# Performance work log

Measured on AMD Instinct MI355X. Metric: run time of the kernel, lower is better.

## Reference

```python
import jax, jax.numpy as jnp
import numpy as np

IMG_H, IMG_W = 240, 320
NEAR, FAR = 0.1, 10.0
CHUNK = 64  # triangles rasterized per scan step
CAM_K = np.array([[286.2057, 0.0, 162.6306],
                  [0.0, 286.7852, 121.0245],
                  [0.0, 0.0, 1.0]], np.float32)


def build_projection(cam, w, h, x0=0, y0=0, nc=NEAR, fc=FAR):
    q = -(fc + nc) / float(fc - nc)
    qn = -2.0 * fc * nc / float(fc - nc)
    proj = np.array([
        [2 * cam[0, 0] / w, -2 * cam[0, 1] / w, (-2 * cam[0, 2] + w + 2 * x0) / w, 0],
        [0, -2 * cam[1, 1] / h, (-2 * cam[1, 2] + h + 2 * y0) / h, 0],
        [0, 0, q, qn],
        [0, 0, -1, 0]], dtype=np.float64)
    proj[1, :] *= -1.0
    return jnp.asarray(proj.T, jnp.float32)


def vertex_normals(verts, faces):
    # per-face normal scattered to its vertices then renormalized
    # (equals dirt lighting.vertex_normals_pre_split on split meshes)
    v0, v1, v2 = verts[faces[:, 0]], verts[faces[:, 1]], verts[faces[:, 2]]
    fn = jnp.cross(v1 - v0, v2 - v0)
    fn = fn / jnp.maximum(jnp.linalg.norm(fn, axis=1, keepdims=True), 1e-12)
    vn = (jnp.zeros_like(verts)
          .at[faces[:, 0]].add(fn)
          .at[faces[:, 1]].add(fn)
          .at[faces[:, 2]].add(fn))
    return vn / jnp.maximum(jnp.linalg.norm(vn, axis=1, keepdims=True), 1e-12)


def transform_vertices(vertices, pose, faces, proj):
    vert_obj = jnp.concatenate([vertices, jnp.ones_like(vertices[:, -1:])], axis=1)  # [V,4]
    normals = vertex_normals(vert_obj[:, :3], faces)
    gl = jnp.array([[1., 0., 0.], [0., -1., 0.], [0., 0., -1.]], jnp.float32)
    rot = gl @ pose[:3, :3]
    # replicate the flat-list surgery: cam_pose[:3,:3]=gl@R, negate t_y, t_z
    cam_pose = pose.at[:3, :3].set(rot).at[1, 3].multiply(-1.0).at[2, 3].multiply(-1.0)
    view = cam_pose.T
    vert_cam = vert_obj @ view                                   # [V,4]
    vert_3d = vert_obj[:, :3] @ pose[:3, :3].T + pose[:3, 3]     # [V,3]
    vert_clip = vert_cam @ proj                                  # [V,4]
    return vert_obj, vert_3d, vert_clip, normals


def rasterise(vert_clip, colors, faces, H, W):
    # z-buffered triangle rasterization with perspective-correct barycentric
    # interpolation, processed in chunks of CHUNK triangles via lax.scan.
    eps = 1e-9
    wc = vert_clip[:, 3]
    inv_w = 1.0 / jnp.where(jnp.abs(wc) > eps, wc, eps)
    ndc = vert_clip[:, :3] * inv_w[:, None]
    px = (ndc[:, 0] + 1.0) * 0.5 * W   # screen x
    py = (1.0 - ndc[:, 1]) * 0.5 * H   # screen y (row 0 at top)
    pz = ndc[:, 2]

    tpx, tpy, tpz = px[faces], py[faces], pz[faces]   # [F,3]
    tiw = inv_w[faces]                                # [F,3]
    tcol = colors[faces]                              # [F,3,C]
    tval = jnp.all(wc[faces] > 1e-6, axis=1)          # all verts in front

    F = faces.shape[0]
    pad = (-F) % CHUNK
    def padf(a):
        if pad == 0:
            return a
        return jnp.concatenate([a, jnp.zeros((pad,) + a.shape[1:], a.dtype)], 0)
    tpx, tpy, tpz, tiw, tcol = padf(tpx), padf(tpy), padf(tpz), padf(tiw), padf(tcol)
    tval = padf(tval)
    n_steps = (F + pad) // CHUNK
    resh = lambda a: a.reshape((n_steps, CHUNK) + a.shape[1:])
    xs = tuple(map(resh, (tpx, tpy, tpz, tiw, tcol, tval)))

    Xg = (jnp.arange(W, dtype=jnp.float32) + 0.5)[None, :, None]  # pixel centers
    Yg = (jnp.arange(H, dtype=jnp.float32) + 0.5)[:, None, None]
    BIG = jnp.float32(1e9)

    def step(carry, chunk):
        zbuf, cbuf = carry
        cpx, cpy, cpz, ciw, ccol, cval = chunk
        ax, ay = cpx[:, 0], cpy[:, 0]
        bx, by = cpx[:, 1], cpy[:, 1]
        cx, cy = cpx[:, 2], cpy[:, 2]
        area = (bx - ax) * (cy - ay) - (by - ay) * (cx - ax)            # [Fc]
        inv_area = 1.0 / jnp.where(jnp.abs(area) > 1e-12, area, 1e-12)
        # normalized edge functions (barycentrics), [H,W,Fc]
        e0 = ((Xg - bx) * (cy - by) - (Yg - by) * (cx - bx)) * inv_area
        e1 = ((Xg - cx) * (ay - cy) - (Yg - cy) * (ax - cx)) * inv_area
        e2 = 1.0 - e0 - e1
        depth = e0 * cpz[:, 0] + e1 * cpz[:, 1] + e2 * cpz[:, 2]        # screen-linear z
        inside = ((e0 >= 0) & (e1 >= 0) & (e2 >= 0) & cval
                  & (jnp.abs(area) > 1e-12) & (depth >= -1.0) & (depth <= 1.0))
        dmask = jnp.where(inside, depth, BIG)
        best = jnp.argmin(dmask, axis=2)                                # [H,W]
        bidx = best[..., None]
        bdepth = jnp.take_along_axis(dmask, bidx, 2)[..., 0]
        take = bdepth < zbuf
        b0 = jnp.take_along_axis(e0, bidx, 2)[..., 0]
        b1 = jnp.take_along_axis(e1, bidx, 2)[..., 0]
        b2 = 1.0 - b0 - b1
        piw = jnp.stack([b0, b1, b2], -1) * ciw[best]                   # [H,W,3]
        den = jnp.sum(piw, -1, keepdims=True)
        den = jnp.where(jnp.abs(den) > 1e-12, den, 1e-12)
        col = jnp.einsum('hwk,hwkc->hwc', piw / den, ccol[best])        # persp-correct
        zbuf = jnp.where(take, bdepth, zbuf)
        cbuf = jnp.where(take[..., None], col, cbuf)
        return (zbuf, cbuf), None

    zbuf0 = jnp.full((H, W), BIG, jnp.float32)
    cbuf0 = jnp.zeros((H, W, colors.shape[1]), jnp.float32)
    (_, cbuf), _ = jax.lax.scan(jax.checkpoint(step), (zbuf0, cbuf0), xs)
    return cbuf


def setup_inputs() -> dict:
    key = jax.random.key(0)
    k1, k2 = jax.random.split(key)
    V, F = 12288, 4096
    vertices = 0.15 * jax.random.normal(k1, (1, V, 3), jnp.float32)
    faces = jax.random.randint(k2, (1, F, 3), 0, V, jnp.int32)
    pose = jnp.eye(4, dtype=jnp.float32).at[2, 3].set(0.6)  # object 0.6m in front
    return {"vertices": vertices, "faces": faces, "poses": pose[None]}


def reference(vertices, faces, poses):
    proj = build_projection(CAM_K, IMG_W, IMG_H)
    faces0 = jnp.asarray(faces[0], jnp.int32)
    vert_obj, vert_3d, vert_clip, normals = transform_vertices(vertices[0], poses[0], faces0, proj)
    colors = jnp.concatenate(
        [jnp.ones_like(vert_obj[:, :1]), vert_3d, normals, vert_obj], axis=1)  # [V,11]
    g = rasterise(vert_clip, colors, faces0, IMG_H, IMG_W)  # [H,W,11]
    return g[None]
```

## Files before the change

kernel.cpp:

```cpp
#include <hip/hip_runtime.h>
#include <math.h>

#pragma clang fp contract(off)

#define IMG_H 240
#define IMG_W 320
#define NPX   (IMG_H * IMG_W)
#define NCH   11
#define NSLICE 8
#define CULL_M 1e-3f

struct ProjM { float m[16]; };

extern "C" __global__ void k_init(float* __restrict__ vnacc, int n3v,
                                  unsigned long long* __restrict__ zkey) {
  int i = blockIdx.x * 256 + threadIdx.x;
  if (i < n3v) vnacc[i] = 0.0f;
  if (i < NPX) zkey[i] = ~0ull;
}

extern "C" __global__ void k_facenorm(const float* __restrict__ verts,
                                      const int* __restrict__ faces,
                                      float* __restrict__ vnacc, int F) {
  int f = blockIdx.x * 256 + threadIdx.x;
  if (f >= F) return;
  int i0 = faces[3*f+0], i1 = faces[3*f+1], i2 = faces[3*f+2];
  float x0 = verts[3*i0+0], y0 = verts[3*i0+1], z0 = verts[3*i0+2];
  float x1 = verts[3*i1+0], y1 = verts[3*i1+1], z1 = verts[3*i1+2];
  float x2 = verts[3*i2+0], y2 = verts[3*i2+1], z2 = verts[3*i2+2];
  float ux = x1 - x0, uy = y1 - y0, uz = z1 - z0;
  float vx = x2 - x0, vy = y2 - y0, vz = z2 - z0;
  float fx = uy*vz - uz*vy;
  float fy = uz*vx - ux*vz;
  float fz = ux*vy - uy*vx;
  float n = sqrtf((fx*fx + fy*fy) + fz*fz);
  float d = fmaxf(n, 1e-12f);
  fx = fx / d; fy = fy / d; fz = fz / d;
  atomicAdd(&vnacc[3*i0+0], fx); atomicAdd(&vnacc[3*i0+1], fy); atomicAdd(&vnacc[3*i0+2], fz);
  atomicAdd(&vnacc[3*i1+0], fx); atomicAdd(&vnacc[3*i1+1], fy); atomicAdd(&vnacc[3*i1+2], fz);
  atomicAdd(&vnacc[3*i2+0], fx); atomicAdd(&vnacc[3*i2+1], fy); atomicAdd(&vnacc[3*i2+2], fz);
}

extern "C" __global__ void k_vertex(const float* __restrict__ verts,
                                    const float* __restrict__ vnacc,
                                    const float* __restrict__ pose,
                                    ProjM P,
                                    float4* __restrict__ pppw,
                                    float* __restrict__ wcb,
                                    float* __restrict__ colors, int V) {
  int i = blockIdx.x * 256 + threadIdx.x;
  if (i >= V) return;
  float x = verts[3*i+0], y = verts[3*i+1], z = verts[3*i+2];

  float nx = vnacc[3*i+0], ny = vnacc[3*i+1], nz = vnacc[3*i+2];
  float nn = sqrtf((nx*nx + ny*ny) + nz*nz);
  float nm = fmaxf(nn, 1e-12f);
  nx = nx / nm; ny = ny / nm; nz = nz / nm;

  float v3x = ((x*pose[0] + y*pose[1]) + z*pose[2])  + pose[3];
  float v3y = ((x*pose[4] + y*pose[5]) + z*pose[6])  + pose[7];
  float v3z = ((x*pose[8] + y*pose[9]) + z*pose[10]) + pose[11];

  float c0 = ((x*pose[0]     + y*pose[1])     + z*pose[2])     + pose[3];
  float c1 = ((x*(-pose[4])  + y*(-pose[5]))  + z*(-pose[6]))  + (-pose[7]);
  float c2 = ((x*(-pose[8])  + y*(-pose[9]))  + z*(-pose[10])) + (-pose[11]);
  float c3 = ((x*pose[12]    + y*pose[13])    + z*pose[14])    + pose[15];

  float q0 = ((c0*P.m[0]  + c1*P.m[1])  + c2*P.m[2])  + c3*P.m[3];
  float q1 = ((c0*P.m[4]  + c1*P.m[5])  + c2*P.m[6])  + c3*P.m[7];
  float q2 = ((c0*P.m[8]  + c1*P.m[9])  + c2*P.m[10]) + c3*P.m[11];
  float q3 = ((c0*P.m[12] + c1*P.m[13]) + c2*P.m[14]) + c3*P.m[15];

  float wc = q3;
  float denw = (fabsf(wc) > 1e-9f) ? wc : 1e-9f;
  float iw = 1.0f / denw;
  float ndx = q0 * iw, ndy = q1 * iw, ndz = q2 * iw;
  float px = ((ndx + 1.0f) * 0.5f) * (float)IMG_W;
  float py = ((1.0f - ndy) * 0.5f) * (float)IMG_H;

  pppw[i] = make_float4(px, py, ndz, iw);
  wcb[i] = wc;

  float* c = colors + (size_t)i * NCH;
  c[0] = 1.0f;
  c[1] = v3x; c[2] = v3y; c[3] = v3z;
  c[4] = nx;  c[5] = ny;  c[6] = nz;
  c[7] = x;   c[8] = y;   c[9] = z; c[10] = 1.0f;
}

extern "C" __global__ void k_facesetup(const int* __restrict__ faces,
                                       const float4* __restrict__ pppw,
                                       const float* __restrict__ wcb,
                                       float4* __restrict__ frec,
                                       float4* __restrict__ fbb,
                                       float4* __restrict__ fe, int F) {
  int f = blockIdx.x * 256 + threadIdx.x;
  if (f >= F) return;
  int i0 = faces[3*f+0], i1 = faces[3*f+1], i2 = faces[3*f+2];
  float4 p0 = pppw[i0], p1 = pppw[i1], p2 = pppw[i2];
  float w0 = wcb[i0], w1 = wcb[i1], w2 = wcb[i2];
  float ax = p0.x, ay = p0.y;
  float bx = p1.x, by = p1.y;
  float cx = p2.x, cy = p2.y;
  float area = (bx - ax) * (cy - ay) - (by - ay) * (cx - ax);
  float inva = 1.0f / ((fabsf(area) > 1e-12f) ? area : 1e-12f);
  bool valid = (w0 > 1e-6f) && (w1 > 1e-6f) && (w2 > 1e-6f) && (fabsf(area) > 1e-12f);
  float rax = 2.0f*cx - ax, ray = 2.0f*cy - ay;
  float rbx = 2.0f*cx - bx, rby = 2.0f*cy - by;
  float minx = fminf(cx, fminf(rax, rbx)), maxx = fmaxf(cx, fmaxf(rax, rbx));
  float miny = fminf(cy, fminf(ray, rby)), maxy = fmaxf(cy, fmaxf(ray, rby));
  frec[4*f+0] = make_float4(bx, by, cy - by, cx - bx);
  frec[4*f+1] = make_float4(cx, cy, ay - cy, ax - cx);
  frec[4*f+2] = make_float4(inva, p0.z, p1.z, p2.z);
  frec[4*f+3] = make_float4(p0.w, p1.w, p2.w, 0.0f);
  fbb[f] = valid ? make_float4(minx, maxx, miny, maxy)
                 : make_float4(1e30f, -1e30f, 1e30f, -1e30f);
  {
    double dbx = bx, dby = by, dcx = cx, dcy = cy, dax = ax, day = ay;
    double dinv = (double)inva;
    double d0 = dcy - dby, d1 = dcx - dbx;
    double d2 = day - dcy, d3 = dax - dcx;
    double a0 = d0 * dinv, b0 = -d1 * dinv, c0 = (dby * d1 - dbx * d0) * dinv;
    double a1 = d2 * dinv, b1 = -d3 * dinv, c1 = (dcy * d3 - dcx * d2) * dinv;
    fe[2*f+0] = make_float4((float)a0, (float)b0, (float)c0, 0.0f);
    fe[2*f+1] = make_float4((float)a1, (float)b1, (float)c1, 0.0f);
  }
}

extern "C" __global__ __launch_bounds__(256)
void k_rasterA(const float4* __restrict__ frec,
               const float4* __restrict__ fbb,
               const float4* __restrict__ fe,
               unsigned long long* __restrict__ zkey,
               int F, int nslice) {
  int t = threadIdx.x;
  int wave = t >> 6;
  int lane = t & 63;
  int sx = (wave & 1) * 8, sy = (wave >> 1) * 8;
  int pxi = blockIdx.x * 16 + sx + (lane & 7);
  int pyi = blockIdx.y * 16 + sy + (lane >> 3);
  float X = (float)pxi + 0.5f;
  float Y = (float)pyi + 0.5f;
  float tXlo = (float)(blockIdx.x * 16 + sx) + 0.5f, tXhi = tXlo + 7.0f;
  float tYlo = (float)(blockIdx.y * 16 + sy) + 0.5f, tYhi = tYlo + 7.0f;

  int f0 = blockIdx.z * nslice;
  int f1 = min(F, f0 + nslice);

  float bestd = 1e9f;
  int   besti = -1;

  for (int base = f0; base < f1; base += 64) {
    int f = base + lane;
    bool ov = false;
    if (f < f1) {
      float4 bb = fbb[f];
      ov = (bb.x - 1.0f <= tXhi) && (bb.y + 1.0f >= tXlo) &&
           (bb.z - 1.0f <= tYhi) && (bb.w + 1.0f >= tYlo);
      if (ov) {
        float4 E0 = fe[2*f+0];
        float4 E1 = fe[2*f+1];
        float pa0 = E0.x * tXlo, pb0 = E0.x * tXhi;
        float qa0 = E0.y * tYlo, qb0 = E0.y * tYhi;
        float e0mx = (fmaxf(pa0, pb0) + fmaxf(qa0, qb0)) + E0.z;
        float e0mn = (fminf(pa0, pb0) + fminf(qa0, qb0)) + E0.z;
        float pa1 = E1.x * tXlo, pb1 = E1.x * tXhi;
        float qa1 = E1.y * tYlo, qb1 = E1.y * tYhi;
        float e1mx = (fmaxf(pa1, pb1) + fmaxf(qa1, qb1)) + E1.z;
        float e1mn = (fminf(pa1, pb1) + fminf(qa1, qb1)) + E1.z;
        float e2mx = (1.0f - e0mn) - e1mn;
        ov = (e0mx >= -CULL_M) && (e1mx >= -CULL_M) && (e2mx >= -CULL_M);
      }
    }
    unsigned long long mask = __ballot(ov);

    while (mask) {
      int j = __builtin_ctzll(mask);
      mask &= mask - 1;
      int ju = __builtin_amdgcn_readfirstlane(base + j);
      const float4* fr = frec + (size_t)ju * 4;
      float4 A = fr[0];
      float4 B = fr[1];
      float4 C = fr[2];
      float t0 = (X - A.x) * A.z;
      float t1 = (Y - A.y) * A.w;
      float e0 = (t0 - t1) * C.x;
      float t2 = (X - B.x) * B.z;
      float t3 = (Y - B.y) * B.w;
      float e1 = (t2 - t3) * C.x;
      float e2 = (1.0f - e0) - e1;
      float depth = ((e0 * C.y) + (e1 * C.z)) + (e2 * C.w);
      bool inside = (e0 >= 0.0f) && (e1 >= 0.0f) && (e2 >= 0.0f) &&
                    (depth >= -1.0f) && (depth <= 1.0f);
      if (inside && depth < bestd) {
        bestd = depth; besti = base + j;
      }
    }
  }

  if (besti >= 0) {
    unsigned int ub = __float_as_uint(bestd);
    ub = (ub & 0x80000000u) ? ~ub : (ub | 0x80000000u);
    unsigned long long key = ((unsigned long long)ub << 32) | (unsigned int)besti;
    atomicMin(&zkey[(size_t)pyi * IMG_W + pxi], key);
  }
}

extern "C" __global__ __launch_bounds__(256)
void k_resolve(const unsigned long long* __restrict__ zkey,
               const float4* __restrict__ frec,
               const float* __restrict__ colors,
               const int* __restrict__ faces,
               float* __restrict__ out) {
  __shared__ float sOut[256 * NCH];
  int t = threadIdx.x;
  int p = blockIdx.x * 256 + t;
  int pyi = p / IMG_W, pxi = p - pyi * IMG_W;
  float X = (float)pxi + 0.5f;
  float Y = (float)pyi + 0.5f;
  unsigned long long key = zkey[p];

  float oc[NCH];
  if (key != ~0ull) {
    int besti = (int)(key & 0xFFFFFFFFu);
    const float4* fr = frec + (size_t)besti * 4;
    float4 A = fr[0], B = fr[1], C = fr[2], D = fr[3];
    float t0 = (X - A.x) * A.z;
    float t1 = (Y - A.y) * A.w;
    float e0 = (t0 - t1) * C.x;
    float t2 = (X - B.x) * B.z;
    float t3 = (Y - B.y) * B.w;
    float e1 = (t2 - t3) * C.x;
    float b2 = (1.0f - e0) - e1;
    float p0 = e0 * D.x, p1 = e1 * D.y, p2 = b2 * D.z;
    float den = (p0 + p1) + p2;
    if (!(fabsf(den) > 1e-12f)) den = 1e-12f;
    float u0 = p0 / den, u1 = p1 / den, u2 = p2 / den;
    int i0 = faces[3*besti+0], i1 = faces[3*besti+1], i2 = faces[3*besti+2];
    const float* c0 = colors + (size_t)i0 * NCH;
    const float* c1 = colors + (size_t)i1 * NCH;
    const float* c2 = colors + (size_t)i2 * NCH;
    #pragma unroll
    for (int ch = 0; ch < NCH; ++ch)
      oc[ch] = (u0 * c0[ch] + u1 * c1[ch]) + u2 * c2[ch];
  } else {
    #pragma unroll
    for (int ch = 0; ch < NCH; ++ch) oc[ch] = 0.0f;
  }
  #pragma unroll
  for (int ch = 0; ch < NCH; ++ch) sOut[t * NCH + ch] = oc[ch];
  __syncthreads();
  float4* o4 = (float4*)(out + (size_t)blockIdx.x * 256 * NCH);
  const float4* s4 = (const float4*)sOut;
  #pragma unroll
  for (int k = 0; k < 3; ++k) {
    int idx = t + k * 256;
    if (idx < 704) o4[idx] = s4[idx];
  }
}

extern "C" void kernel_launch(void* const* d_in, const int* in_sizes, int n_in,
                              void* d_out, int out_size, void* d_ws, size_t ws_size,
                              hipStream_t stream) {
  const float* verts = (const float*)d_in[0];
  const int*   faces = (const int*)d_in[1];
  const float* pose  = (const float*)d_in[2];
  float* out = (float*)d_out;
  int V = in_sizes[0] / 3;
  int F = in_sizes[1] / 3;

  float* ws = (float*)d_ws;
  size_t o = 0;
  auto alloc = [&](size_t n) { size_t r = o; o += (n + 3) & ~(size_t)3; return r; };
  size_t o_zk   = alloc((size_t)2 * NPX);
  size_t o_vn   = alloc((size_t)3 * V);
  size_t o_pppw = alloc((size_t)4 * V);
  size_t o_wc   = alloc((size_t)V);
  size_t o_col  = alloc((size_t)NCH * V);
  size_t o_fr   = alloc((size_t)16 * F);
  size_t o_bb   = alloc((size_t)4 * F);
  size_t o_fe   = alloc((size_t)8 * F);
  unsigned long long* zkey = (unsigned long long*)(ws + o_zk);
  float*  vnacc = ws + o_vn;
  float4* pppw  = (float4*)(ws + o_pppw);
  float*  wcb   = ws + o_wc;
  float*  col   = ws + o_col;
  float4* frec  = (float4*)(ws + o_fr);
  float4* fbb   = (float4*)(ws + o_bb);
  float4* fe    = (float4*)(ws + o_fe);

  double fxd = 286.2057, sd = 0.0, cxd = 162.6306;
  double fyd = 286.7852, cyd = 121.0245;
  double wd = IMG_W, hd = IMG_H, ncd = 0.1, fcd = 10.0;
  double q  = -(fcd + ncd) / (fcd - ncd);
  double qn = -2.0 * fcd * ncd / (fcd - ncd);
  double Pd[16] = {
    2.0*fxd/wd, -2.0*sd/wd, (-2.0*cxd + wd)/wd, 0.0,
    0.0,        2.0*fyd/hd, (2.0*cyd - hd)/hd, -0.0,
    0.0,        0.0,        q,                  qn,
    0.0,        0.0,       -1.0,                0.0 };
  ProjM P;
  for (int i = 0; i < 16; ++i) P.m[i] = (float)Pd[i];

  int n3v = 3 * V;
  int initN = (NPX > n3v) ? NPX : n3v;
  k_init<<<(initN + 255) / 256, 256, 0, stream>>>(vnacc, n3v, zkey);
  k_facenorm<<<(F + 255) / 256, 256, 0, stream>>>(verts, faces, vnacc, F);
  k_vertex<<<(V + 255) / 256, 256, 0, stream>>>(verts, vnacc, pose, P, pppw, wcb, col, V);
  k_facesetup<<<(F + 255) / 256, 256, 0, stream>>>(faces, pppw, wcb, frec, fbb, fe, F);
  int nslice = (F + NSLICE - 1) / NSLICE;
  dim3 g(IMG_W / 16, IMG_H / 16, NSLICE);
  k_rasterA<<<g, 256, 0, stream>>>(frec, fbb, fe, zkey, F, nslice);
  k_resolve<<<NPX / 256, 256, 0, stream>>>(zkey, frec, col, faces, out);
}
```

Before: 98.49 us.

## Fuse face normal and setup kernels, add depth early-out, pad colors to float4

New measurement: 91.02 us, median of 3. 7.6% less time.

```diff
diff --git a/kernel.cpp b/kernel.cpp
--- a/kernel.cpp
+++ b/kernel.cpp
@@ -7,8 +7,10 @@
 #define IMG_W 320
 #define NPX   (IMG_H * IMG_W)
 #define NCH   11
+#define NCHP  12
 #define NSLICE 8
 #define CULL_M 1e-3f
+#define EZ_M   1e-5f
 
 struct ProjM { float m[16]; };
 
@@ -19,89 +21,62 @@
   if (i < NPX) zkey[i] = ~0ull;
 }
 
-extern "C" __global__ void k_facenorm(const float* __restrict__ verts,
-                                      const int* __restrict__ faces,
-                                      float* __restrict__ vnacc, int F) {
-  int f = blockIdx.x * 256 + threadIdx.x;
+__device__ __forceinline__ void xform(float x, float y, float z,
+                                      const float* __restrict__ pose,
+                                      const ProjM& P,
+                                      float& px, float& py, float& pz,
+                                      float& iw, float& wc) {
+  float c0 = ((x*pose[0]     + y*pose[1])     + z*pose[2])     + pose[3];
+  float c1 = ((x*(-pose[4])  + y*(-pose[5]))  + z*(-pose[6]))  + (-pose[7]);
+  float c2 = ((x*(-pose[8])  + y*(-pose[9]))  + z*(-pose[10])) + (-pose[11]);
+  float c3 = ((x*pose[12]    + y*pose[13])    + z*pose[14])    + pose[15];
+  float q0 = ((c0*P.m[0]  + c1*P.m[1])  + c2*P.m[2])  + c3*P.m[3];
+  float q1 = ((c0*P.m[4]  + c1*P.m[5])  + c2*P.m[6])  + c3*P.m[7];
+  float q2 = ((c0*P.m[8]  + c1*P.m[9])  + c2*P.m[10]) + c3*P.m[11];
+  float q3 = ((c0*P.m[12] + c1*P.m[13]) + c2*P.m[14]) + c3*P.m[15];
+  wc = q3;
+  float denw = (fabsf(wc) > 1e-9f) ? wc : 1e-9f;
+  iw = 1.0f / denw;
+  float ndx = q0 * iw, ndy = q1 * iw;
+  pz = q2 * iw;
+  px = ((ndx + 1.0f) * 0.5f) * (float)IMG_W;
+  py = ((1.0f - ndy) * 0.5f) * (float)IMG_H;
+}
+
+extern "C" __global__ void k_face(const float* __restrict__ verts,
+                                  const int* __restrict__ faces,
+                                  const float* __restrict__ pose,
+                                  ProjM P,
+                                  float* __restrict__ vnacc,
+                                  float4* __restrict__ frec,
+                                  float4* __restrict__ fbb,
+                                  float4* __restrict__ fe,
+                                  int4*  __restrict__ fidx, int F) {
+  int f = blockIdx.x * 64 + threadIdx.x;
   if (f >= F) return;
   int i0 = faces[3*f+0], i1 = faces[3*f+1], i2 = faces[3*f+2];
   float x0 = verts[3*i0+0], y0 = verts[3*i0+1], z0 = verts[3*i0+2];
   float x1 = verts[3*i1+0], y1 = verts[3*i1+1], z1 = verts[3*i1+2];
   float x2 = verts[3*i2+0], y2 = verts[3*i2+1], z2 = verts[3*i2+2];
-  float ux = x1 - x0, uy = y1 - y0, uz = z1 - z0;
-  float vx = x2 - x0, vy = y2 - y0, vz = z2 - z0;
-  float fx = uy*vz - uz*vy;
-  float fy = uz*vx - ux*vz;
-  float fz = ux*vy - uy*vx;
-  float n = sqrtf((fx*fx + fy*fy) + fz*fz);
-  float d = fmaxf(n, 1e-12f);
-  fx = fx / d; fy = fy / d; fz = fz / d;
-  atomicAdd(&vnacc[3*i0+0], fx); atomicAdd(&vnacc[3*i0+1], fy); atomicAdd(&vnacc[3*i0+2], fz);
-  atomicAdd(&vnacc[3*i1+0], fx); atomicAdd(&vnacc[3*i1+1], fy); atomicAdd(&vnacc[3*i1+2], fz);
-  atomicAdd(&vnacc[3*i2+0], fx); atomicAdd(&vnacc[3*i2+1], fy); atomicAdd(&vnacc[3*i2+2], fz);
-}
-
-extern "C" __global__ void k_vertex(const float* __restrict__ verts,
-                                    const float* __restrict__ vnacc,
-                                    const float* __restrict__ pose,
-                                    ProjM P,
-                                    float4* __restrict__ pppw,
-                                    float* __restrict__ wcb,
-                                    float* __restrict__ colors, int V) {
-  int i = blockIdx.x * 256 + threadIdx.x;
-  if (i >= V) return;
-  float x = verts[3*i+0], y = verts[3*i+1], z = verts[3*i+2];
-
-  float nx = vnacc[3*i+0], ny = vnacc[3*i+1], nz = vnacc[3*i+2];
-  float nn = sqrtf((nx*nx + ny*ny) + nz*nz);
-  float nm = fmaxf(nn, 1e-12f);
-  nx = nx / nm; ny = ny / nm; nz = nz / nm;
-
-  float v3x = ((x*pose[0] + y*pose[1]) + z*pose[2])  + pose[3];
-  float v3y = ((x*pose[4] + y*pose[5]) + z*pose[6])  + pose[7];
-  float v3z = ((x*pose[8] + y*pose[9]) + z*pose[10]) + pose[11];
-
-  float c0 = ((x*pose[0]     + y*pose[1])     + z*pose[2])     + pose[3];
-  float c1 = ((x*(-pose[4])  + y*(-pose[5]))  + z*(-pose[6]))  + (-pose[7]);
-  float c2 = ((x*(-pose[8])  + y*(-pose[9]))  + z*(-pose[10])) + (-pose[11]);
-  float c3 = ((x*pose[12]    + y*pose[13])    + z*pose[14])    + pose[15];
-
-  float q0 = ((c0*P.m[0]  + c1*P.m[1])  + c2*P.m[2])  + c3*P.m[3];
-  float q1 = ((c0*P.m[4]  + c1*P.m[5])  + c2*P.m[6])  + c3*P.m[7];
-  float q2 = ((c0*P.m[8]  + c1*P.m[9])  + c2*P.m[10]) + c3*P.m[11];
-  float q3 = ((c0*P.m[12] + c1*P.m[13]) + c2*P.m[14]) + c3*P.m[15];
-
-  float wc = q3;
-  float denw = (fabsf(wc) > 1e-9f) ? wc : 1e-9f;
-  float iw = 1.0f / denw;
-  float ndx = q0 * iw, ndy = q1 * iw, ndz = q2 * iw;
-  float px = ((ndx + 1.0f) * 0.5f) * (float)IMG_W;
-  float py = ((1.0f - ndy) * 0.5f) * (float)IMG_H;
-
-  pppw[i] = make_float4(px, py, ndz, iw);
-  wcb[i] = wc;
-
-  float* c = colors + (size_t)i * NCH;
-  c[0] = 1.0f;
-  c[1] = v3x; c[2] = v3y; c[3] = v3z;
-  c[4] = nx;  c[5] = ny;  c[6] = nz;
-  c[7] = x;   c[8] = y;   c[9] = z; c[10] = 1.0f;
-}
-
-extern "C" __global__ void k_facesetup(const int* __restrict__ faces,
-                                       const float4* __restrict__ pppw,
-                                       const float* __restrict__ wcb,
-                                       float4* __restrict__ frec,
-                                       float4* __restrict__ fbb,
-                                       float4* __restrict__ fe, int F) {
-  int f = blockIdx.x * 256 + threadIdx.x;
-  if (f >= F) return;
-  int i0 = faces[3*f+0], i1 = faces[3*f+1], i2 = faces[3*f+2];
-  float4 p0 = pppw[i0], p1 = pppw[i1], p2 = pppw[i2];
-  float w0 = wcb[i0], w1 = wcb[i1], w2 = wcb[i2];
-  float ax = p0.x, ay = p0.y;
-  float bx = p1.x, by = p1.y;
-  float cx = p2.x, cy = p2.y;
+
+  {
+    float ux = x1 - x0, uy = y1 - y0, uz = z1 - z0;
+    float vx = x2 - x0, vy = y2 - y0, vz = z2 - z0;
+    float fx = uy*vz - uz*vy;
+    float fy = uz*vx - ux*vz;
+    float fz = ux*vy - uy*vx;
+    float n = sqrtf((fx*fx + fy*fy) + fz*fz);
+    float d = fmaxf(n, 1e-12f);
+    fx = fx / d; fy = fy / d; fz = fz / d;
+    atomicAdd(&vnacc[3*i0+0], fx); atomicAdd(&vnacc[3*i0+1], fy); atomicAdd(&vnacc[3*i0+2], fz);
+    atomicAdd(&vnacc[3*i1+0], fx); atomicAdd(&vnacc[3*i1+1], fy); atomicAdd(&vnacc[3*i1+2], fz);
+    atomicAdd(&vnacc[3*i2+0], fx); atomicAdd(&vnacc[3*i2+1], fy); atomicAdd(&vnacc[3*i2+2], fz);
+  }
+
+  float ax, ay, pz0, iw0, w0;  xform(x0, y0, z0, pose, P, ax, ay, pz0, iw0, w0);
+  float bx, by, pz1, iw1, w1;  xform(x1, y1, z1, pose, P, bx, by, pz1, iw1, w1);
+  float cx, cy, pz2, iw2, w2;  xform(x2, y2, z2, pose, P, cx, cy, pz2, iw2, w2);
+
   float area = (bx - ax) * (cy - ay) - (by - ay) * (cx - ax);
   float inva = 1.0f / ((fabsf(area) > 1e-12f) ? area : 1e-12f);
   bool valid = (w0 > 1e-6f) && (w1 > 1e-6f) && (w2 > 1e-6f) && (fabsf(area) > 1e-12f);
@@ -111,10 +86,11 @@
   float miny = fminf(cy, fminf(ray, rby)), maxy = fmaxf(cy, fmaxf(ray, rby));
   frec[4*f+0] = make_float4(bx, by, cy - by, cx - bx);
   frec[4*f+1] = make_float4(cx, cy, ay - cy, ax - cx);
-  frec[4*f+2] = make_float4(inva, p0.z, p1.z, p2.z);
-  frec[4*f+3] = make_float4(p0.w, p1.w, p2.w, 0.0f);
+  frec[4*f+2] = make_float4(inva, pz0, pz1, pz2);
+  frec[4*f+3] = make_float4(iw0, iw1, iw2, 0.0f);
   fbb[f] = valid ? make_float4(minx, maxx, miny, maxy)
                  : make_float4(1e30f, -1e30f, 1e30f, -1e30f);
+  fidx[f] = make_int4(i0, i1, i2, 0);
   {
     double dbx = bx, dby = by, dcx = cx, dcy = cy, dax = ax, day = ay;
     double dinv = (double)inva;
@@ -125,6 +101,28 @@
     fe[2*f+0] = make_float4((float)a0, (float)b0, (float)c0, 0.0f);
     fe[2*f+1] = make_float4((float)a1, (float)b1, (float)c1, 0.0f);
   }
+}
+
+extern "C" __global__ void k_vertex(const float* __restrict__ verts,
+                                    const float* __restrict__ vnacc,
+                                    const float* __restrict__ pose,
+                                    float4* __restrict__ colors, int V) {
+  int i = blockIdx.x * 64 + threadIdx.x;
+  if (i >= V) return;
+  float x = verts[3*i+0], y = verts[3*i+1], z = verts[3*i+2];
+
+  float nx = vnacc[3*i+0], ny = vnacc[3*i+1], nz = vnacc[3*i+2];
+  float nn = sqrtf((nx*nx + ny*ny) + nz*nz);
+  float nm = fmaxf(nn, 1e-12f);
+  nx = nx / nm; ny = ny / nm; nz = nz / nm;
+
+  float v3x = ((x*pose[0] + y*pose[1]) + z*pose[2])  + pose[3];
+  float v3y = ((x*pose[4] + y*pose[5]) + z*pose[6])  + pose[7];
+  float v3z = ((x*pose[8] + y*pose[9]) + z*pose[10]) + pose[11];
+
+  colors[3*i+0] = make_float4(1.0f, v3x, v3y, v3z);
+  colors[3*i+1] = make_float4(nx, ny, nz, x);
+  colors[3*i+2] = make_float4(y, z, 1.0f, 0.0f);
 }
 
 extern "C" __global__ __launch_bounds__(256)
@@ -179,9 +177,11 @@
       mask &= mask - 1;
       int ju = __builtin_amdgcn_readfirstlane(base + j);
       const float4* fr = frec + (size_t)ju * 4;
+      float4 C = fr[2];
+      float zminf = fminf(C.y, fminf(C.z, C.w));
+      if (__ballot(bestd > zminf - EZ_M) == 0ull) continue;
       float4 A = fr[0];
       float4 B = fr[1];
-      float4 C = fr[2];
       float t0 = (X - A.x) * A.z;
       float t1 = (Y - A.y) * A.w;
       float e0 = (t0 - t1) * C.x;
@@ -209,8 +209,8 @@
 extern "C" __global__ __launch_bounds__(256)
 void k_resolve(const unsigned long long* __restrict__ zkey,
                const float4* __restrict__ frec,
-               const float* __restrict__ colors,
-               const int* __restrict__ faces,
+               const float4* __restrict__ colors,
+               const int4* __restrict__ fidx,
                float* __restrict__ out) {
   __shared__ float sOut[256 * NCH];
   int t = threadIdx.x;
@@ -236,13 +236,17 @@
     float den = (p0 + p1) + p2;
     if (!(fabsf(den) > 1e-12f)) den = 1e-12f;
     float u0 = p0 / den, u1 = p1 / den, u2 = p2 / den;
-    int i0 = faces[3*besti+0], i1 = faces[3*besti+1], i2 = faces[3*besti+2];
-    const float* c0 = colors + (size_t)i0 * NCH;
-    const float* c1 = colors + (size_t)i1 * NCH;
-    const float* c2 = colors + (size_t)i2 * NCH;
+    int4 vi = fidx[besti];
+    float c0v[NCHP], c1v[NCHP], c2v[NCHP];
+    #pragma unroll
+    for (int k = 0; k < 3; ++k) {
+      *(float4*)(c0v + 4*k) = colors[3*vi.x + k];
+      *(float4*)(c1v + 4*k) = colors[3*vi.y + k];
+      *(float4*)(c2v + 4*k) = colors[3*vi.z + k];
+    }
     #pragma unroll
     for (int ch = 0; ch < NCH; ++ch)
-      oc[ch] = (u0 * c0[ch] + u1 * c1[ch]) + u2 * c2[ch];
+      oc[ch] = (u0 * c0v[ch] + u1 * c1v[ch]) + u2 * c2v[ch];
   } else {
     #pragma unroll
     for (int ch = 0; ch < NCH; ++ch) oc[ch] = 0.0f;
@@ -274,20 +278,18 @@
   auto alloc = [&](size_t n) { size_t r = o; o += (n + 3) & ~(size_t)3; return r; };
   size_t o_zk   = alloc((size_t)2 * NPX);
   size_t o_vn   = alloc((size_t)3 * V);
-  size_t o_pppw = alloc((size_t)4 * V);
-  size_t o_wc   = alloc((size_t)V);
-  size_t o_col  = alloc((size_t)NCH * V);
+  size_t o_col  = alloc((size_t)NCHP * V);
   size_t o_fr   = alloc((size_t)16 * F);
   size_t o_bb   = alloc((size_t)4 * F);
   size_t o_fe   = alloc((size_t)8 * F);
+  size_t o_fi   = alloc((size_t)4 * F);
   unsigned long long* zkey = (unsigned long long*)(ws + o_zk);
   float*  vnacc = ws + o_vn;
-  float4* pppw  = (float4*)(ws + o_pppw);
-  float*  wcb   = ws + o_wc;
-  float*  col   = ws + o_col;
+  float4* col   = (float4*)(ws + o_col);
   float4* frec  = (float4*)(ws + o_fr);
   float4* fbb   = (float4*)(ws + o_bb);
   float4* fe    = (float4*)(ws + o_fe);
+  int4*   fidx  = (int4*)(ws + o_fi);
 
   double fxd = 286.2057, sd = 0.0, cxd = 162.6306;
   double fyd = 286.7852, cyd = 121.0245;
@@ -305,11 +307,11 @@
   int n3v = 3 * V;
   int initN = (NPX > n3v) ? NPX : n3v;
   k_init<<<(initN + 255) / 256, 256, 0, stream>>>(vnacc, n3v, zkey);
-  k_facenorm<<<(F + 255) / 256, 256, 0, stream>>>(verts, faces, vnacc, F);
-  k_vertex<<<(V + 255) / 256, 256, 0, stream>>>(verts, vnacc, pose, P, pppw, wcb, col, V);
-  k_facesetup<<<(F + 255) / 256, 256, 0, stream>>>(faces, pppw, wcb, frec, fbb, fe, F);
+  k_face<<<(F + 63) / 64, 64, 0, stream>>>(verts, faces, pose, P, vnacc,
+                                           frec, fbb, fe, fidx, F);
+  k_vertex<<<(V + 63) / 64, 64, 0, stream>>>(verts, vnacc, pose, col, V);
   int nslice = (F + NSLICE - 1) / NSLICE;
   dim3 g(IMG_W / 16, IMG_H / 16, NSLICE);
   k_rasterA<<<g, 256, 0, stream>>>(frec, fbb, fe, zkey, F, nslice);
-  k_resolve<<<NPX / 256, 256, 0, stream>>>(zkey, frec, col, faces, out);
-}
+  k_resolve<<<NPX / 256, 256, 0, stream>>>(zkey, frec, col, fidx, out);
+}
```
